# Optimization experiments

Hardware: AMD Instinct MI355X
Metric: run time of the kernel (lower is better)

## Reference

```python
import jax, jax.numpy as jnp
import numpy as np

B, C, H, W = 32, 256, 32, 32
K, HEADS, U, V = 16, 4, 1, 64  # dim_depth, heads, dim_u, dim_v = dim_out//heads
R = 23
PAD = (R - 1) // 2
EPS = 1e-5


def setup_inputs() -> dict:
    key = jax.random.key(0)
    ks = jax.random.split(key, 10)
    return {
        "x": jax.random.normal(ks[0], (B, C, H, W), jnp.float32),
        "Wq": jax.random.normal(ks[1], (K * HEADS, C), jnp.float32) * (1.0 / np.sqrt(C)),
        "bn_q_w": jax.random.uniform(ks[2], (K * HEADS,), jnp.float32, 0.5, 1.5),
        "bn_q_b": jax.random.normal(ks[3], (K * HEADS,), jnp.float32) * 0.1,
        "Wk": jax.random.normal(ks[4], (K * U, C), jnp.float32) * (1.0 / np.sqrt(C)),
        "Wv": jax.random.normal(ks[5], (V * U, C), jnp.float32) * (1.0 / np.sqrt(C)),
        "bn_v_w": jax.random.uniform(ks[6], (V * U,), jnp.float32, 0.5, 1.5),
        "bn_v_b": jax.random.normal(ks[7], (V * U,), jnp.float32) * 0.1,
        "embedding": jax.random.normal(ks[8], (K, U, 1, R, R), jnp.float32),
        "gamma": jax.random.normal(ks[9], (1,), jnp.float32),
    }


def _conv1x1(x, w):
    # x: [b,c,h,w], w: [o,c] -> [b,o,h,w]
    return jnp.einsum('bchw,oc->bohw', x, w)


def _bn(x, w, b):
    # training-mode BatchNorm2d: batch stats over (b,h,w) per channel
    mean = jnp.mean(x, axis=(0, 2, 3), keepdims=True)
    var = jnp.var(x, axis=(0, 2, 3), keepdims=True)
    xn = (x - mean) * jax.lax.rsqrt(var + EPS)
    return xn * w[None, :, None, None] + b[None, :, None, None]


def reference(x, Wq, bn_q_w, bn_q_b, Wk, Wv, bn_v_w, bn_v_b, embedding, gamma):
    b, c, h, w = x.shape
    n = h * w
    queries = _bn(_conv1x1(x, Wq), bn_q_w, bn_q_b).reshape(b, HEADS, K, n)        # bhkn
    softmax = jax.nn.softmax(_conv1x1(x, Wk).reshape(b, K, U, n), axis=-1)         # bkun
    values = _bn(_conv1x1(x, Wv), bn_v_w, bn_v_b).reshape(b, V, U, n)              # bvun

    # content lambda
    lambda_c = jnp.einsum('bkun,bvun->bkv', softmax, values)
    y_c = jnp.einsum('bhkn,bkv->bhvn', queries, lambda_c)

    # position lambda via conv3d over (V, H, W) with kernel (1, R, R)
    v5 = jnp.transpose(values, (0, 2, 1, 3)).reshape(b, U, V, h, w)                # NCDHW, C=U, D=V
    lambda_p = jax.lax.conv_general_dilated(
        v5, embedding,
        window_strides=(1, 1, 1),
        padding=((0, 0), (PAD, PAD), (PAD, PAD)),
        dimension_numbers=('NCDHW', 'OIDHW', 'NCDHW'))                              # [b,K,V,h,w]
    lambda_p = lambda_p.reshape(b, K, V, n)
    y_p = jnp.einsum('bhkn,bkvn->bhvn', queries, lambda_p)

    out = (y_c + y_p).reshape(b, HEADS * V, h, w)
    out = out + gamma * out
    return out
```

## Files before the change

kernel.cpp:

```cpp
#include <hip/hip_runtime.h>
#include <math.h>

#define BB 32
#define CC 256
#define NPIX 1024
#define KD 16
#define NHEADS 4
#define VDIM 64
#define RR 23
#define PADR 11
#define EPSBN 1e-5f

typedef short short8v __attribute__((ext_vector_type(8)));
typedef short short4v __attribute__((ext_vector_type(4)));
typedef float floatx4 __attribute__((ext_vector_type(4)));

__device__ __forceinline__ unsigned short f2bf(float f) {
  union { float f; unsigned u; } c; c.f = f;
  unsigned u = c.u;
  return (unsigned short)((u + 0x7FFFu + ((u >> 16) & 1u)) >> 16);
}
__device__ __forceinline__ float bf2f(unsigned short h) {
  union { unsigned u; float f; } c; c.u = ((unsigned)h) << 16;
  return c.f;
}

#define NINV (1.0f / 32768.0f)

__global__ __launch_bounds__(256) void k_prep(const float* __restrict__ emb,
    unsigned short* __restrict__ embA,
    const float* __restrict__ Wq, const float* __restrict__ Wk,
    const float* __restrict__ Wv, unsigned short* __restrict__ wA,
    float* __restrict__ raw) {
  int bid = blockIdx.x;
  if (bid == 0) raw[threadIdx.x] = 0.f;
  if (bid < 46) {
    int l = bid * 256 + threadIdx.x;
    if (l >= 23 * 16 * 32) return;
    int dr = l >> 9, rem = l & 511;
    int m = rem >> 5, kd = rem & 31;
    unsigned short val = 0;
    if (kd < 23) val = f2bf(emb[(size_t)m * 529 + dr * 23 + kd]);
    embA[l] = val;
  } else {
    int idx = (bid - 46) * 256 + threadIdx.x;
    int j = idx & 7, lane = (idx >> 3) & 63, ks = (idx >> 9) & 7, ot = idx >> 12;
    int o = ot * 16 + (lane & 15);
    int c = ks * 32 + (lane >> 4) * 8 + j;
    const float* src = (o < 64) ? (Wq + (size_t)o * CC)
                     : (o < 80) ? (Wk + (size_t)(o - 64) * CC)
                                : (Wv + (size_t)(o - 80) * CC);
    wA[idx] = f2bf(src[c]);
  }
}

__global__ __launch_bounds__(256) void k_proj(const float* __restrict__ x,
    const unsigned short* __restrict__ wA,
    float* __restrict__ q_pre, float* __restrict__ k_pre, float* __restrict__ v_pre,
    float* __restrict__ raw) {
  __shared__ float ssum[144], ssq[144];
  int b = blockIdx.y;
  int t = threadIdx.x;
  int s = t >> 6;
  int lane = t & 63;
  int nl = lane & 15, quad = lane >> 4;
  int pix = blockIdx.x * 64 + s * 16 + nl;

  if (t < 144) { ssum[t] = 0.f; ssq[t] = 0.f; }
  __syncthreads();

  const float* xb = x + ((size_t)b * CC) * NPIX + pix;
  const unsigned short* ap = wA + lane * 8;

  floatx4 acc[9];
#pragma unroll
  for (int i = 0; i < 9; ++i) acc[i] = (floatx4){0.f, 0.f, 0.f, 0.f};

#pragma unroll
  for (int ks = 0; ks < 8; ++ks) {
    union { short8v v; unsigned short u[8]; } bb;
    const float* xc = xb + ((size_t)(ks * 32 + quad * 8)) * NPIX;
#pragma unroll
    for (int j = 0; j < 8; ++j) bb.u[j] = f2bf(xc[(size_t)j * NPIX]);
#pragma unroll
    for (int ot = 0; ot < 9; ++ot) {
      short8v af = *(const short8v*)(ap + ((ot * 8 + ks) << 9));
      acc[ot] = __builtin_amdgcn_mfma_f32_16x16x32_bf16(af, bb.v, acc[ot], 0, 0, 0);
    }
  }

#pragma unroll
  for (int ot = 0; ot < 9; ++ot) {
#pragma unroll
    for (int r = 0; r < 4; ++r) {
      int o = ot * 16 + quad * 4 + r;
      float val = acc[ot][r];
      if (o < 64)      q_pre[((size_t)b * 64 + o) * NPIX + pix] = val;
      else if (o < 80) k_pre[((size_t)b * 16 + (o - 64)) * NPIX + pix] = val;
      else             v_pre[((size_t)b * 64 + (o - 80)) * NPIX + pix] = val;
    }
  }

#pragma unroll
  for (int ot = 0; ot < 9; ++ot) {
#pragma unroll
    for (int r = 0; r < 4; ++r) {
      int o = ot * 16 + quad * 4 + r;
      if (o >= 64 && o < 80) continue;
      float v1 = acc[ot][r];
      float v2 = v1 * v1;
#pragma unroll
      for (int m = 1; m < 16; m <<= 1) {
        v1 += __shfl_xor(v1, m);
        v2 += __shfl_xor(v2, m);
      }
      if (nl == 0) {
        atomicAdd(&ssum[o], v1);
        atomicAdd(&ssq[o], v2);
      }
    }
  }
  __syncthreads();
  if (t < 64) {
    atomicAdd(&raw[t], ssum[t]);
    atomicAdd(&raw[64 + t], ssq[t]);
  } else if (t < 128) {
    atomicAdd(&raw[64 + t], ssum[t + 16]);
    atomicAdd(&raw[192 + (t - 64)], ssq[t + 16]);
  }
}

__global__ __launch_bounds__(256) void k_nvsm(float* __restrict__ vn,
    const float* __restrict__ raw,
    const float* __restrict__ bn_v_w, const float* __restrict__ bn_v_b,
    const float* __restrict__ k_pre, float* __restrict__ p) {
  __shared__ float vsc[64], vsh[64];
  __shared__ float shm[4], shs[4];
  int b = blockIdx.y, bx = blockIdx.x, t = threadIdx.x;
  if (bx < 16) {
    if (t < 64) {
      float mean = raw[128 + t] * NINV;
      float var = raw[192 + t] * NINV - mean * mean;
      float sc = rsqrtf(var + EPSBN) * bn_v_w[t];
      vsc[t] = sc;
      vsh[t] = bn_v_b[t] - mean * sc;
    }
    __syncthreads();
    int n0 = bx * 64;
    for (int l = t; l < 4096; l += 256) {
      int o = l >> 6, nn = l & 63;
      size_t a = ((size_t)b * 64 + o) * NPIX + n0 + nn;
      vn[a] = fmaf(vn[a], vsc[o], vsh[o]);
    }
  } else {
    int k = bx - 16;
    const float* src = k_pre + ((size_t)b * 16 + k) * NPIX;
    float v[4];
    float mx = -1e30f;
#pragma unroll
    for (int i = 0; i < 4; ++i) { v[i] = src[t + 256 * i]; mx = fmaxf(mx, v[i]); }
#pragma unroll
    for (int off = 32; off > 0; off >>= 1) mx = fmaxf(mx, __shfl_down(mx, off));
    if ((t & 63) == 0) shm[t >> 6] = mx;
    __syncthreads();
    mx = fmaxf(fmaxf(shm[0], shm[1]), fmaxf(shm[2], shm[3]));
    float s = 0.f;
#pragma unroll
    for (int i = 0; i < 4; ++i) { v[i] = __expf(v[i] - mx); s += v[i]; }
#pragma unroll
    for (int off = 32; off > 0; off >>= 1) s += __shfl_down(s, off);
    if ((t & 63) == 0) shs[t >> 6] = s;
    __syncthreads();
    float r = 1.0f / (shs[0] + shs[1] + shs[2] + shs[3]);
    float* dst = p + ((size_t)b * 16 + k) * NPIX;
#pragma unroll
    for (int i = 0; i < 4; ++i) dst[t + 256 * i] = v[i] * r;
  }
}

#define IMG_RS 68
#define IMG_CS 3728
#define LAM_RS 1032

union KMainLDS {
  short imgc[4 * IMG_CS];
  short lam[16 * LAM_RS];
};

__device__ __forceinline__ short8v ld_win(const short* p) {
  union { short8v s8; short4v s4[2]; } bu;
  bu.s4[0] = *(const short4v*)p;
  bu.s4[1] = *(const short4v*)(p + 4);
  return bu.s8;
}

__global__ __launch_bounds__(256, 3) void k_conv(const float* __restrict__ vn,
    const float* __restrict__ p, const unsigned short* __restrict__ embA,
    unsigned short* __restrict__ lamG) {
  __shared__ __align__(16) KMainLDS u;
  __shared__ float lcv[16];
  __shared__ float red[64];
  int b = blockIdx.y, v = blockIdx.x, t = threadIdx.x;
  int lane = t & 63, wv = t >> 6;

  int4* z4 = (int4*)u.imgc;
  for (int l = t; l < 1864; l += 256) z4[l] = make_int4(0, 0, 0, 0);
  __syncthreads();

  const float* vsrc = vn + ((size_t)b * 64 + v) * NPIX;
  const float* psrc = p + (size_t)b * 16 * NPIX;
  float part[16];
#pragma unroll
  for (int k = 0; k < 16; ++k) part[k] = 0.f;

  for (int l = t; l < 512; l += 256) {
    int pix = l * 2;
    int y = pix >> 5, xx = pix & 31;
    float2 vv = *(const float2*)(vsrc + pix);
    unsigned short h0 = f2bf(vv.x), h1 = f2bf(vv.y);
#pragma unroll
    for (int s = 0; s < 4; ++s) {
      int base = s * IMG_CS + (y + PADR) * IMG_RS + xx + PADR + s;
      u.imgc[base] = (short)h0;
      u.imgc[base + 1] = (short)h1;
    }
#pragma unroll
    for (int k = 0; k < 16; ++k) {
      float2 pk = *(const float2*)(psrc + (size_t)k * NPIX + pix);
      part[k] = fmaf(pk.x, vv.x, fmaf(pk.y, vv.y, part[k]));
    }
  }
#pragma unroll
  for (int k = 0; k < 16; ++k) {
#pragma unroll
    for (int m = 1; m < 64; m <<= 1) part[k] += __shfl_xor(part[k], m);
  }
  if (lane == 0) {
#pragma unroll
    for (int k = 0; k < 16; ++k) red[wv * 16 + k] = part[k];
  }
  __syncthreads();
  if (t < 16)
    lcv[t] = red[t] + red[16 + t] + red[32 + t] + red[48 + t];

  int nl = lane & 15, quad = lane >> 4;
  int y0 = wv * 8;
  int scopy = (4 - (nl & 3)) & 3;
  int colbase = scopy * IMG_CS + nl + quad * 8 + scopy;
  const unsigned short* aptr = embA + nl * 32 + quad * 8;

  floatx4 acc[16];
#pragma unroll
  for (int i = 0; i < 16; ++i) acc[i] = (floatx4){0.f, 0.f, 0.f, 0.f};

  short8v bfrag[8][2];
#pragma unroll
  for (int rr = 0; rr < 8; ++rr) {
    const short* rp = &u.imgc[(y0 + rr) * IMG_RS + colbase];
    bfrag[rr][0] = ld_win(rp);
    bfrag[rr][1] = ld_win(rp + 16);
  }

  short8v a0 = *(const short8v*)aptr;
  short8v a1 = *(const short8v*)(aptr + 512);
#pragma unroll
  for (int dr = 0; dr < RR; ++dr) {
    short8v afrag = a0;
    a0 = a1;
    if (dr < RR - 2) a1 = *(const short8v*)(aptr + (dr + 2) * 512);
#pragma unroll
    for (int rr = 0; rr < 8; ++rr) {
      int slot = (dr + rr) & 7;
      acc[rr * 2 + 0] = __builtin_amdgcn_mfma_f32_16x16x32_bf16(afrag, bfrag[slot][0], acc[rr * 2 + 0], 0, 0, 0);
      acc[rr * 2 + 1] = __builtin_amdgcn_mfma_f32_16x16x32_bf16(afrag, bfrag[slot][1], acc[rr * 2 + 1], 0, 0, 0);
    }
    if (dr < RR - 1) {
      const short* rp = &u.imgc[(y0 + dr + 8) * IMG_RS + colbase];
      int slot = dr & 7;
      bfrag[slot][0] = ld_win(rp);
      bfrag[slot][1] = ld_win(rp + 16);
    }
  }

  __syncthreads();
#pragma unroll
  for (int tt = 0; tt < 16; ++tt) {
    int y = y0 + (tt >> 1), c0 = (tt & 1) << 4;
    int pix = y * 32 + c0 + nl;
#pragma unroll
    for (int r = 0; r < 4; ++r)
      u.lam[(quad * 4 + r) * LAM_RS + pix] = (short)f2bf(acc[tt][r] + lcv[quad * 4 + r]);
  }
  __syncthreads();

  uint4* dst = (uint4*)(lamG + ((size_t)(b * 64 + v)) * 16 * 1024);
  for (int idx = t; idx < 2048; idx += 256) {
    int row = idx >> 7, col = idx & 127;
    dst[row * 128 + col] = *(const uint4*)&u.lam[row * LAM_RS + col * 8];
  }
}

__global__ __launch_bounds__(256) void k_epi2(const unsigned short* __restrict__ lamG,
    const float* __restrict__ q_pre, const float* __restrict__ raw,
    const float* __restrict__ bn_q_w, const float* __restrict__ bn_q_b,
    const float* __restrict__ gamma, float* __restrict__ out) {
  __shared__ float qs[64 * 64];
  __shared__ float qsc[64], qsh[64];
  int b = blockIdx.y, nc = blockIdx.x, z = blockIdx.z, t = threadIdx.x;
  if (t < 64) {
    float mean = raw[t] * NINV;
    float var = raw[64 + t] * NINV - mean * mean;
    float sc = rsqrtf(var + EPSBN) * bn_q_w[t];
    qsc[t] = sc;
    qsh[t] = bn_q_b[t] - mean * sc;
  }
  __syncthreads();
  int n0 = nc * 64;
  for (int l = t; l < 4096; l += 256) {
    int o = l >> 6, nn = l & 63;
    qs[l] = fmaf(q_pre[((size_t)b * 64 + o) * NPIX + n0 + nn], qsc[o], qsh[o]);
  }
  __syncthreads();
  float g1 = 1.0f + gamma[0];
  int p0 = (t & 15) * 4;
  int g = t >> 4;
#pragma unroll
  for (int vi = 0; vi < 2; ++vi) {
    int v = z * 32 + vi * 16 + g;
    const unsigned short* ls = lamG + ((size_t)(b * 64 + v)) * 16 * 1024 + n0 + p0;
    float yacc[4][4];
#pragma unroll
    for (int h = 0; h < 4; ++h)
#pragma unroll
      for (int i = 0; i < 4; ++i) yacc[h][i] = 0.f;
#pragma unroll
    for (int k = 0; k < 16; ++k) {
      uint2 w = *(const uint2*)(ls + k * 1024);
      float l0 = bf2f((unsigned short)(w.x & 0xffffu));
      float l1 = bf2f((unsigned short)(w.x >> 16));
      float l2 = bf2f((unsigned short)(w.y & 0xffffu));
      float l3 = bf2f((unsigned short)(w.y >> 16));
#pragma unroll
      for (int h = 0; h < 4; ++h) {
        const float* qrow = &qs[(h * 16 + k) * 64 + p0];
        yacc[h][0] = fmaf(qrow[0], l0, yacc[h][0]);
        yacc[h][1] = fmaf(qrow[1], l1, yacc[h][1]);
        yacc[h][2] = fmaf(qrow[2], l2, yacc[h][2]);
        yacc[h][3] = fmaf(qrow[3], l3, yacc[h][3]);
      }
    }
#pragma unroll
    for (int h = 0; h < 4; ++h) {
      float4 r;
      r.x = g1 * yacc[h][0]; r.y = g1 * yacc[h][1];
      r.z = g1 * yacc[h][2]; r.w = g1 * yacc[h][3];
      *(float4*)&out[((size_t)b * 256 + h * 64 + v) * NPIX + n0 + p0] = r;
    }
  }
}

__global__ __launch_bounds__(256, 3) void k_fused(const float* __restrict__ vn,
    const float* __restrict__ q_pre, const float* __restrict__ raw,
    const float* __restrict__ bn_q_w, const float* __restrict__ bn_q_b,
    const float* __restrict__ p, const unsigned short* __restrict__ embA,
    const float* __restrict__ gamma, float* __restrict__ out) {
  __shared__ __align__(16) KMainLDS u;
  __shared__ float lcv[16];
  __shared__ float red[256];
  __shared__ float qsc[64], qsh[64];
  int b = blockIdx.y, v = blockIdx.x, t = threadIdx.x;

  int4* z4 = (int4*)u.imgc;
  for (int l = t; l < 1864; l += 256) z4[l] = make_int4(0, 0, 0, 0);
  if (t < 64) {
    float mean = raw[t] * NINV;
    float var = raw[64 + t] * NINV - mean * mean;
    float sc = rsqrtf(var + EPSBN) * bn_q_w[t];
    qsc[t] = sc;
    qsh[t] = bn_q_b[t] - mean * sc;
  }
  {
    int kk = t & 15, ch = t >> 4;
    const float* pp = p + ((size_t)b * 16 + kk) * NPIX + ch * 64;
    const float* vv = vn + ((size_t)b * 64 + v) * NPIX + ch * 64;
    float part = 0.f;
#pragma unroll 8
    for (int i = 0; i < 64; ++i) part = fmaf(pp[i], vv[i], part);
    red[t] = part;
  }
  __syncthreads();
  if (t < 16) {
    float s = 0.f;
#pragma unroll
    for (int c = 0; c < 16; ++c) s += red[c * 16 + t];
    lcv[t] = s;
  }

  const float* vsrc = vn + ((size_t)b * 64 + v) * NPIX;
  for (int l = t; l < 512; l += 256) {
    int pix = l * 2;
    int y = pix >> 5, xx = pix & 31;
    float2 vv = *(const float2*)(vsrc + pix);
    unsigned short h0 = f2bf(vv.x), h1 = f2bf(vv.y);
#pragma unroll
    for (int s = 0; s < 4; ++s) {
      int base = s * IMG_CS + (y + PADR) * IMG_RS + xx + PADR + s;
      u.imgc[base] = (short)h0;
      u.imgc[base + 1] = (short)h1;
    }
  }
  __syncthreads();

  int lane = t & 63, wv = t >> 6;
  int nl = lane & 15, quad = lane >> 4;
  int y0 = wv * 8;
  int scopy = (4 - (nl & 3)) & 3;
  int colbase = scopy * IMG_CS + nl + quad * 8 + scopy;
  const unsigned short* aptr = embA + nl * 32 + quad * 8;

  floatx4 acc[16];
#pragma unroll
  for (int i = 0; i < 16; ++i) acc[i] = (floatx4){0.f, 0.f, 0.f, 0.f};

  short8v bfrag[8][2];
#pragma unroll
  for (int rr = 0; rr < 8; ++rr) {
    const short* rp = &u.imgc[(y0 + rr) * IMG_RS + colbase];
    bfrag[rr][0] = ld_win(rp);
    bfrag[rr][1] = ld_win(rp + 16);
  }

  short8v a0 = *(const short8v*)aptr;
  short8v a1 = *(const short8v*)(aptr + 512);
#pragma unroll
  for (int dr = 0; dr < RR; ++dr) {
    short8v afrag = a0;
    a0 = a1;
    if (dr < RR - 2) a1 = *(const short8v*)(aptr + (dr + 2) * 512);
#pragma unroll
    for (int rr = 0; rr < 8; ++rr) {
      int slot = (dr + rr) & 7;
      acc[rr * 2 + 0] = __builtin_amdgcn_mfma_f32_16x16x32_bf16(afrag, bfrag[slot][0], acc[rr * 2 + 0], 0, 0, 0);
      acc[rr * 2 + 1] = __builtin_amdgcn_mfma_f32_16x16x32_bf16(afrag, bfrag[slot][1], acc[rr * 2 + 1], 0, 0, 0);
    }
    if (dr < RR - 1) {
      const short* rp = &u.imgc[(y0 + dr + 8) * IMG_RS + colbase];
      int slot = dr & 7;
      bfrag[slot][0] = ld_win(rp);
      bfrag[slot][1] = ld_win(rp + 16);
    }
  }

  __syncthreads();
#pragma unroll
  for (int tt = 0; tt < 16; ++tt) {
    int y = y0 + (tt >> 1), c0 = (tt & 1) << 4;
    int pix = y * 32 + c0 + nl;
#pragma unroll
    for (int r = 0; r < 4; ++r)
      u.lam[(quad * 4 + r) * LAM_RS + pix] = (short)f2bf(acc[tt][r] + lcv[quad * 4 + r]);
  }
  __syncthreads();

  int p0 = t * 4;
  float yacc[4][4];
#pragma unroll
  for (int h = 0; h < 4; ++h)
#pragma unroll
    for (int i = 0; i < 4; ++i) yacc[h][i] = 0.f;
  const float* qb = q_pre + ((size_t)b * 64) * NPIX + p0;
#pragma unroll
  for (int k = 0; k < 16; ++k) {
    uint2 w = *(const uint2*)&u.lam[k * LAM_RS + p0];
    float l0 = bf2f((unsigned short)(w.x & 0xffffu));
    float l1 = bf2f((unsigned short)(w.x >> 16));
    float l2 = bf2f((unsigned short)(w.y & 0xffffu));
    float l3 = bf2f((unsigned short)(w.y >> 16));
#pragma unroll
    for (int h = 0; h < 4; ++h) {
      int o = h * 16 + k;
      float4 qv = *(const float4*)(qb + (size_t)o * NPIX);
      yacc[h][0] = fmaf(fmaf(qv.x, qsc[o], qsh[o]), l0, yacc[h][0]);
      yacc[h][1] = fmaf(fmaf(qv.y, qsc[o], qsh[o]), l1, yacc[h][1]);
      yacc[h][2] = fmaf(fmaf(qv.z, qsc[o], qsh[o]), l2, yacc[h][2]);
      yacc[h][3] = fmaf(fmaf(qv.w, qsc[o], qsh[o]), l3, yacc[h][3]);
    }
  }
  float g1 = 1.0f + gamma[0];
#pragma unroll
  for (int h = 0; h < 4; ++h) {
    float4 r;
    r.x = g1 * yacc[h][0]; r.y = g1 * yacc[h][1];
    r.z = g1 * yacc[h][2]; r.w = g1 * yacc[h][3];
    *(float4*)&out[((size_t)b * 256 + h * 64 + v) * NPIX + p0] = r;
  }
}

extern "C" void kernel_launch(void* const* d_in, const int* in_sizes, int n_in,
                              void* d_out, int out_size, void* d_ws, size_t ws_size,
                              hipStream_t stream) {
  const float* x      = (const float*)d_in[0];
  const float* Wq     = (const float*)d_in[1];
  const float* bn_q_w = (const float*)d_in[2];
  const float* bn_q_b = (const float*)d_in[3];
  const float* Wk     = (const float*)d_in[4];
  const float* Wv     = (const float*)d_in[5];
  const float* bn_v_w = (const float*)d_in[6];
  const float* bn_v_b = (const float*)d_in[7];
  const float* emb    = (const float*)d_in[8];
  const float* gamma  = (const float*)d_in[9];
  float* out = (float*)d_out;

  float* ws    = (float*)d_ws;
  float* q_pre = ws;
  float* k_pre = q_pre + (size_t)BB * 64 * NPIX;
  float* vn    = k_pre + (size_t)BB * 16 * NPIX;
  float* p     = vn    + (size_t)BB * 64 * NPIX;
  float* raw   = p     + (size_t)BB * 16 * NPIX;
  unsigned short* embA = (unsigned short*)(raw + 256);
  unsigned short* wA   = embA + 23 * 16 * 32;
  unsigned short* lamG = wA + 144 * 256;

  size_t need = ((size_t)(lamG - (unsigned short*)ws)) * 2
              + (size_t)BB * 64 * 16 * NPIX * 2;

  k_prep  <<<dim3(190),       256, 0, stream>>>(emb, embA, Wq, Wk, Wv, wA, raw);
  k_proj  <<<dim3(16, BB),    256, 0, stream>>>(x, wA, q_pre, k_pre, vn, raw);
  k_nvsm  <<<dim3(32, BB),    256, 0, stream>>>(vn, raw, bn_v_w, bn_v_b, k_pre, p);
  if (ws_size >= need) {
    k_conv<<<dim3(64, BB),    256, 0, stream>>>(vn, p, embA, lamG);
    k_epi2<<<dim3(16, BB, 2), 256, 0, stream>>>(lamG, q_pre, raw, bn_q_w, bn_q_b, gamma, out);
  } else {
    k_fused<<<dim3(64, BB),   256, 0, stream>>>(vn, q_pre, raw, bn_q_w, bn_q_b, p, embA, gamma, out);
  }
}
```

Baseline: 208.8 us.

## Split content-lambda reduction into separate conv blocks, add it in epilogue

```diff
diff --git a/kernel.cpp b/kernel.cpp
--- a/kernel.cpp
+++ b/kernel.cpp
@@ -196,23 +196,51 @@
 
 __global__ __launch_bounds__(256, 3) void k_conv(const float* __restrict__ vn,
     const float* __restrict__ p, const unsigned short* __restrict__ embA,
-    unsigned short* __restrict__ lamG) {
+    unsigned short* __restrict__ lamG, float* __restrict__ lcG) {
   __shared__ __align__(16) KMainLDS u;
-  __shared__ float lcv[16];
-  __shared__ float red[64];
-  int b = blockIdx.y, v = blockIdx.x, t = threadIdx.x;
+  __shared__ float red2[256];
+  int b = blockIdx.y, bx = blockIdx.x, t = threadIdx.x;
   int lane = t & 63, wv = t >> 6;
 
+  if (bx >= 64) {
+    int kk = bx - 64;
+    const float* pk = p + ((size_t)b * 16 + kk) * NPIX;
+    const float* vb = vn + (size_t)b * 64 * NPIX;
+    float pr[4];
+#pragma unroll
+    for (int i = 0; i < 4; ++i) pr[i] = pk[t + 256 * i];
+    float part[64];
+#pragma unroll
+    for (int v64 = 0; v64 < 64; ++v64) part[v64] = 0.f;
+#pragma unroll
+    for (int v64 = 0; v64 < 64; ++v64) {
+      const float* vr = vb + (size_t)v64 * NPIX + t;
+#pragma unroll
+      for (int i = 0; i < 4; ++i)
+        part[v64] = fmaf(pr[i], vr[256 * i], part[v64]);
+    }
+#pragma unroll
+    for (int v64 = 0; v64 < 64; ++v64) {
+#pragma unroll
+      for (int m = 1; m < 64; m <<= 1) part[v64] += __shfl_xor(part[v64], m);
+    }
+    if (lane == 0) {
+#pragma unroll
+      for (int v64 = 0; v64 < 64; ++v64) red2[wv * 64 + v64] = part[v64];
+    }
+    __syncthreads();
+    if (t < 64)
+      lcG[(size_t)b * 1024 + kk * 64 + t] =
+          red2[t] + red2[64 + t] + red2[128 + t] + red2[192 + t];
+    return;
+  }
+
+  int v = bx;
   int4* z4 = (int4*)u.imgc;
   for (int l = t; l < 1864; l += 256) z4[l] = make_int4(0, 0, 0, 0);
   __syncthreads();
 
   const float* vsrc = vn + ((size_t)b * 64 + v) * NPIX;
-  const float* psrc = p + (size_t)b * 16 * NPIX;
-  float part[16];
-#pragma unroll
-  for (int k = 0; k < 16; ++k) part[k] = 0.f;
-
   for (int l = t; l < 512; l += 256) {
     int pix = l * 2;
     int y = pix >> 5, xx = pix & 31;
@@ -224,24 +252,8 @@
       u.imgc[base] = (short)h0;
       u.imgc[base + 1] = (short)h1;
     }
-#pragma unroll
-    for (int k = 0; k < 16; ++k) {
-      float2 pk = *(const float2*)(psrc + (size_t)k * NPIX + pix);
-      part[k] = fmaf(pk.x, vv.x, fmaf(pk.y, vv.y, part[k]));
-    }
-  }
-#pragma unroll
-  for (int k = 0; k < 16; ++k) {
-#pragma unroll
-    for (int m = 1; m < 64; m <<= 1) part[k] += __shfl_xor(part[k], m);
-  }
-  if (lane == 0) {
-#pragma unroll
-    for (int k = 0; k < 16; ++k) red[wv * 16 + k] = part[k];
-  }
-  __syncthreads();
-  if (t < 16)
-    lcv[t] = red[t] + red[16 + t] + red[32 + t] + red[48 + t];
+  }
+  __syncthreads();
 
   int nl = lane & 15, quad = lane >> 4;
   int y0 = wv * 8;
@@ -289,7 +301,7 @@
     int pix = y * 32 + c0 + nl;
 #pragma unroll
     for (int r = 0; r < 4; ++r)
-      u.lam[(quad * 4 + r) * LAM_RS + pix] = (short)f2bf(acc[tt][r] + lcv[quad * 4 + r]);
+      u.lam[(quad * 4 + r) * LAM_RS + pix] = (short)f2bf(acc[tt][r]);
   }
   __syncthreads();
 
@@ -303,8 +315,10 @@
 __global__ __launch_bounds__(256) void k_epi2(const unsigned short* __restrict__ lamG,
     const float* __restrict__ q_pre, const float* __restrict__ raw,
     const float* __restrict__ bn_q_w, const float* __restrict__ bn_q_b,
+    const float* __restrict__ lcG,
     const float* __restrict__ gamma, float* __restrict__ out) {
   __shared__ float qs[64 * 64];
+  __shared__ float lcs[1024];
   __shared__ float qsc[64], qsh[64];
   int b = blockIdx.y, nc = blockIdx.x, z = blockIdx.z, t = threadIdx.x;
   if (t < 64) {
@@ -314,6 +328,7 @@
     qsc[t] = sc;
     qsh[t] = bn_q_b[t] - mean * sc;
   }
+  for (int l = t; l < 1024; l += 256) lcs[l] = lcG[(size_t)b * 1024 + l];
   __syncthreads();
   int n0 = nc * 64;
   for (int l = t; l < 4096; l += 256) {
@@ -336,10 +351,11 @@
 #pragma unroll
     for (int k = 0; k < 16; ++k) {
       uint2 w = *(const uint2*)(ls + k * 1024);
-      float l0 = bf2f((unsigned short)(w.x & 0xffffu));
-      float l1 = bf2f((unsigned short)(w.x >> 16));
-      float l2 = bf2f((unsigned short)(w.y & 0xffffu));
-      float l3 = bf2f((unsigned short)(w.y >> 16));
+      float lv = lcs[k * 64 + v];
+      float l0 = bf2f((unsigned short)(w.x & 0xffffu)) + lv;
+      float l1 = bf2f((unsigned short)(w.x >> 16)) + lv;
+      float l2 = bf2f((unsigned short)(w.y & 0xffffu)) + lv;
+      float l3 = bf2f((unsigned short)(w.y >> 16)) + lv;
 #pragma unroll
       for (int h = 0; h < 4; ++h) {
         const float* qrow = &qs[(h * 16 + k) * 64 + p0];
@@ -517,7 +533,8 @@
   float* vn    = k_pre + (size_t)BB * 16 * NPIX;
   float* p     = vn    + (size_t)BB * 64 * NPIX;
   float* raw   = p     + (size_t)BB * 16 * NPIX;
-  unsigned short* embA = (unsigned short*)(raw + 256);
+  float* lcG   = raw + 256;
+  unsigned short* embA = (unsigned short*)(lcG + (size_t)BB * 1024);
   unsigned short* wA   = embA + 23 * 16 * 32;
   unsigned short* lamG = wA + 144 * 256;
 
@@ -528,8 +545,8 @@
   k_proj  <<<dim3(16, BB),    256, 0, stream>>>(x, wA, q_pre, k_pre, vn, raw);
   k_nvsm  <<<dim3(32, BB),    256, 0, stream>>>(vn, raw, bn_v_w, bn_v_b, k_pre, p);
   if (ws_size >= need) {
-    k_conv<<<dim3(64, BB),    256, 0, stream>>>(vn, p, embA, lamG);
-    k_epi2<<<dim3(16, BB, 2), 256, 0, stream>>>(lamG, q_pre, raw, bn_q_w, bn_q_b, gamma, out);
+    k_conv<<<dim3(80, BB),    256, 0, stream>>>(vn, p, embA, lamG, lcG);
+    k_epi2<<<dim3(16, BB, 2), 256, 0, stream>>>(lamG, q_pre, raw, bn_q_w, bn_q_b, lcG, gamma, out);
   } else {
     k_fused<<<dim3(64, BB),   256, 0, stream>>>(vn, q_pre, raw, bn_q_w, bn_q_b, p, embA, gamma, out);
   }
```

Result: slower. 239.7 us (+14.8%).
